# Performance work log

Hardware: AMD Instinct MI355X
Metric: run time of the kernel (lower is better)

The kernel has to match this reference:

```python
import jax, jax.numpy as jnp
import numpy as np

H = 2048          # hidden_size
I_MOE = 1408      # moe_intermediate_size (per expert)
I_SH = 5632       # shared_expert_intermediate_size
E = 8             # num_experts
TOP_K = 2         # num_experts_per_tok
B, S = 1, 2048


def setup_inputs() -> dict:
    key = jax.random.key(0)
    ks = jax.random.split(key, 7)
    sc = 0.02
    return {
        "hidden_states": jax.random.normal(ks[0], (B, S, H), jnp.float32),
        "W_router": jax.random.normal(ks[1], (E, H), jnp.float32) * sc,      # gate.weight
        "W_sgate": jax.random.normal(ks[2], (1, H), jnp.float32) * sc,       # shared_expert_gate.weight
        "Ws_gate_up": jax.random.normal(ks[3], (H, 2 * I_SH), jnp.float32) * sc,  # shared expert merged gate/up
        "Ws_down": jax.random.normal(ks[4], (I_SH, H), jnp.float32) * sc,
        "We_gate_up": jax.random.normal(ks[5], (E, H, 2 * I_MOE), jnp.float32) * sc,  # stacked expert gate/up
        "We_down": jax.random.normal(ks[6], (E, I_MOE, H), jnp.float32) * sc,
    }


def _silu_and_mul(gu, inter):
    # gate_up layout: [..., 2*inter] -> silu(gate) * up, matching SiluAndMul
    return jax.nn.silu(gu[..., :inter]) * gu[..., inter:]


def reference(hidden_states, W_router, W_sgate, Ws_gate_up, Ws_down, We_gate_up, We_down):
    orig_shape = hidden_states.shape
    x = hidden_states.reshape(-1, H)                     # [T, H]
    T = x.shape[0]

    # --- router: softmax in fp32 then top-k (NOT renormalized, as in source) ---
    logits = x @ W_router.T                              # [T, E]
    probs = jax.nn.softmax(logits.astype(jnp.float32), axis=-1)
    rw, sel = jax.lax.top_k(probs, TOP_K)                # [T, K]
    rw = rw.astype(x.dtype)

    # sparse combine matrix [T, E]: routing weight where selected, else 0
    combine = jnp.zeros((T, E), x.dtype).at[jnp.arange(T)[:, None], sel].add(rw)

    # --- shared expert ---
    sh = _silu_and_mul(x @ Ws_gate_up, I_SH) @ Ws_down    # [T, H]
    shared_out = sh * jax.nn.sigmoid(x @ W_sgate.T)       # [T, H]

    # --- experts: dense dispatch (math-identical to gather/MLP/index_add loop) ---
    gu = jnp.einsum('th,ehi->eti', x, We_gate_up)         # [E, T, 2*I_MOE]
    h = _silu_and_mul(gu, I_MOE)                          # [E, T, I_MOE]
    eo = jnp.einsum('eti,eih->eth', h, We_down)           # [E, T, H]
    sparse_out = jnp.einsum('eth,te->th', eo, combine)    # [T, H]

    return (shared_out + sparse_out).reshape(orig_shape)
```

## Files before the change

kernel.cpp:

```cpp
#include <hip/hip_runtime.h>
#include <cstdio>


#define H_DIM 2048
#define IMOE  1408
#define ISH   5632
#define NEXP  8
#define T_TOK 2048
#define TK_TOT (T_TOK * 2)

typedef __attribute__((ext_vector_type(8))) short short8;
typedef __attribute__((ext_vector_type(8))) __bf16 bf16x8;
typedef __attribute__((ext_vector_type(4))) float f32x4;

__device__ __forceinline__ float bf2f(unsigned short u) {
  union { unsigned int i; float f; } v; v.i = ((unsigned int)u) << 16; return v.f;
}
__device__ __forceinline__ unsigned short f2bf(float f) {
  union { float f; unsigned int i; } v; v.f = f;
  unsigned int x = v.i;
  return (unsigned short)((x + 0x7fffu + ((x >> 16) & 1u)) >> 16);
}

__device__ __forceinline__ f32x4 MFMA16(short8 a, short8 b, f32x4 c) {
  return __builtin_amdgcn_mfma_f32_16x16x32_bf16(
      __builtin_bit_cast(bf16x8, a), __builtin_bit_cast(bf16x8, b), c, 0, 0, 0);
}

__device__ __forceinline__ void gload_lds16(const unsigned short* g, unsigned short* l) {
  __builtin_amdgcn_global_load_lds(
      (const __attribute__((address_space(1))) unsigned int*)g,
      (__attribute__((address_space(3))) unsigned int*)l, 16, 0, 0);
}

__device__ __forceinline__ float silu_f(float x) { return x / (1.0f + __expf(-x)); }


__global__ __launch_bounds__(256)
void transpose_cvt_kernel(const float* __restrict__ src, unsigned short* __restrict__ dst,
                          int R, int C, long sStride, long dStride) {
  src += (long)blockIdx.z * sStride;
  dst += (long)blockIdx.z * dStride;
  __shared__ float tile[32][33];
  int tx = threadIdx.x, ty = threadIdx.y;
  int x = blockIdx.x * 32 + tx;
  int yb = blockIdx.y * 32;
#pragma unroll
  for (int j = 0; j < 4; j++) {
    int y = yb + ty + j * 8;
    tile[ty + j * 8][tx] = src[(long)y * C + x];
  }
  __syncthreads();
  int c = blockIdx.x * 32 + ty;
  int r = yb + tx;
#pragma unroll
  for (int j = 0; j < 4; j++) {
    dst[(long)(c + j * 8) * R + r] = f2bf(tile[tx][ty + j * 8]);
  }
}

__global__ __launch_bounds__(256)
void cvt_x_kernel(const float* __restrict__ x, unsigned short* __restrict__ xb, int total4) {
  int i = blockIdx.x * 256 + threadIdx.x;
  if (i >= total4) return;
  float4 v = ((const float4*)x)[i];
  ushort4 o;
  o.x = f2bf(v.x); o.y = f2bf(v.y); o.z = f2bf(v.z); o.w = f2bf(v.w);
  ((ushort4*)xb)[i] = o;
}


__global__ __launch_bounds__(256)
void router_kernel(const float* __restrict__ x, const float* __restrict__ Wr,
                   const float* __restrict__ Wsg, float* __restrict__ rw,
                   int* __restrict__ sel, float* __restrict__ sgate_sig,
                   int* __restrict__ counts) {
  int t = blockIdx.x;
  const float* xr = x + (long)t * H_DIM;
  float p[9];
#pragma unroll
  for (int e = 0; e < 9; e++) p[e] = 0.0f;
  for (int h = threadIdx.x; h < H_DIM; h += 256) {
    float xv = xr[h];
#pragma unroll
    for (int e = 0; e < 8; e++) p[e] += xv * Wr[e * H_DIM + h];
    p[8] += xv * Wsg[h];
  }
#pragma unroll
  for (int e = 0; e < 9; e++)
    for (int off = 32; off > 0; off >>= 1)
      p[e] += __shfl_down(p[e], off, 64);
  __shared__ float red[4][9];
  int wave = threadIdx.x >> 6, lane = threadIdx.x & 63;
  if (lane == 0) {
#pragma unroll
    for (int e = 0; e < 9; e++) red[wave][e] = p[e];
  }
  __syncthreads();
  if (threadIdx.x == 0) {
    float lg[9];
#pragma unroll
    for (int e = 0; e < 9; e++) lg[e] = red[0][e] + red[1][e] + red[2][e] + red[3][e];
    float m = lg[0];
#pragma unroll
    for (int e = 1; e < 8; e++) m = fmaxf(m, lg[e]);
    float pr[8], s = 0.0f;
#pragma unroll
    for (int e = 0; e < 8; e++) { pr[e] = expf(lg[e] - m); s += pr[e]; }
    float inv = 1.0f / s;
#pragma unroll
    for (int e = 0; e < 8; e++) pr[e] *= inv;
    int i0 = 0;
#pragma unroll
    for (int e = 1; e < 8; e++) if (pr[e] > pr[i0]) i0 = e;
    int i1 = (i0 == 0) ? 1 : 0;
#pragma unroll
    for (int e = 0; e < 8; e++) if (e != i0 && pr[e] > pr[i1]) i1 = e;
    rw[t * 2] = pr[i0]; rw[t * 2 + 1] = pr[i1];
    sel[t * 2] = i0;    sel[t * 2 + 1] = i1;
    sgate_sig[t] = 1.0f / (1.0f + expf(-lg[8]));
    atomicAdd(&counts[i0], 1);
    atomicAdd(&counts[i1], 1);
  }
}

__global__ void scan_kernel(const int* __restrict__ counts, int* __restrict__ offsets) {
  if (threadIdx.x == 0 && blockIdx.x == 0) {
    int s = 0;
    for (int e = 0; e < NEXP; e++) { offsets[e] = s; s += counts[e]; }
    offsets[NEXP] = s;
  }
}

__global__ __launch_bounds__(256)
void scatter_kernel(const int* __restrict__ sel, const int* __restrict__ offsets,
                    int* __restrict__ cursor, int* __restrict__ tok_of_slot,
                    int* __restrict__ slot_of_tok) {
  int t = blockIdx.x * 256 + threadIdx.x;
  if (t >= T_TOK) return;
#pragma unroll
  for (int k = 0; k < 2; k++) {
    int e = sel[t * 2 + k];
    int pos = atomicAdd(&cursor[e], 1);
    int slot = offsets[e] + pos;
    tok_of_slot[slot] = t;
    slot_of_tok[t * 2 + k] = slot;
  }
}

template <int EPI, bool EXPERT, bool GATHER>
__global__ __launch_bounds__(256, 2)
void gemm_bt_kernel(const unsigned short* __restrict__ A,
                    const unsigned short* __restrict__ BT,
                    void* __restrict__ Cv, int M, int N, int K,
                    const int* __restrict__ counts, const int* __restrict__ offsets,
                    const int* __restrict__ tok_of_slot,
                    const float* __restrict__ rowscale, long bt_estride) {
  int cnt = M, rowbase = 0;
  if constexpr (EXPERT) {
    int e = blockIdx.z;
    cnt = counts[e];
    rowbase = offsets[e];
    BT += (long)e * bt_estride;
  }
  int row0 = blockIdx.x * 128;
  if (row0 >= cnt) return;
  int col0 = blockIdx.y * 128;

  __shared__ unsigned short As[128 * 32];
  __shared__ unsigned short Bs[128 * 32];

  int tid = threadIdx.x;
  int wave = tid >> 6, lane = tid & 63;

  int c0 = wave * 64 + lane;
  int c1 = c0 + 256;
  int ar0 = c0 >> 2, ak0 = (c0 & 3) * 8;
  int ar1 = c1 >> 2, ak1 = (c1 & 3) * 8;

  long ga0, ga1;
  {
    int r0 = row0 + ar0, r1 = row0 + ar1;
    if constexpr (EXPERT) {
      int s0 = rowbase + min(r0, cnt - 1);
      int s1 = rowbase + min(r1, cnt - 1);
      if constexpr (GATHER) { ga0 = tok_of_slot[s0]; ga1 = tok_of_slot[s1]; }
      else { ga0 = s0; ga1 = s1; }
    } else { ga0 = r0; ga1 = r1; }
  }
  const unsigned short* aS0 = A + ga0 * (long)K + ak0;
  const unsigned short* aS1 = A + ga1 * (long)K + ak1;
  const unsigned short* bS0 = BT + (long)(col0 + ar0) * K + ak0;
  const unsigned short* bS1 = BT + (long)(col0 + ar1) * K + ak1;

  unsigned short* lA0 = &As[wave * 512];
  unsigned short* lA1 = &As[(4 + wave) * 512];
  unsigned short* lB0 = &Bs[wave * 512];
  unsigned short* lB1 = &Bs[(4 + wave) * 512];

  int wr = (wave >> 1) * 64, wc = (wave & 1) * 64;
  int fr = lane & 15, fg = lane >> 4;

  f32x4 acc[4][4] = {};

  for (int k = 0; k < K; k += 32) {
    gload_lds16(aS0 + k, lA0);
    gload_lds16(aS1 + k, lA1);
    gload_lds16(bS0 + k, lB0);
    gload_lds16(bS1 + k, lB1);
    __syncthreads();
    short8 aF[4], bF[4];
#pragma unroll
    for (int m = 0; m < 4; m++)
      aF[m] = *(const short8*)&As[(wr + m * 16 + fr) * 32 + fg * 8];
#pragma unroll
    for (int n = 0; n < 4; n++)
      bF[n] = *(const short8*)&Bs[(wc + n * 16 + fr) * 32 + fg * 8];
#pragma unroll
    for (int m = 0; m < 4; m++)
#pragma unroll
      for (int n = 0; n < 4; n++)
        acc[m][n] = MFMA16(aF[m], bF[n], acc[m][n]);
    __syncthreads();
  }

#pragma unroll
  for (int m = 0; m < 4; m++) {
    int rbase = wr + m * 16 + fg * 4;
#pragma unroll
    for (int n = 0; n < 4; n++) {
      int cg = col0 + wc + n * 16 + fr;
      f32x4 v = acc[m][n];
#pragma unroll
      for (int r = 0; r < 4; r++) {
        int rl = rbase + r;
        if (row0 + rl < cnt) {
          long orow = (long)(EXPERT ? rowbase : 0) + row0 + rl;
          long ci = orow * (long)N + cg;
          if constexpr (EPI == 0)      ((unsigned short*)Cv)[ci] = f2bf(v[r]);
          else if constexpr (EPI == 1) ((float*)Cv)[ci] = v[r] * rowscale[orow];
          else                         ((float*)Cv)[ci] = v[r];
        }
      }
    }
  }
}


__global__ __launch_bounds__(256)
void silu_mul_kernel(const unsigned short* __restrict__ gu, unsigned short* __restrict__ h,
                     int rows, int I) {
  int i = blockIdx.x * 256 + threadIdx.x;
  int i4 = I >> 2;
  if (i >= rows * i4) return;
  int row = i / i4;
  int ci = (i - row * i4) * 4;
  const unsigned short* g = gu + (long)row * 2 * I + ci;
  ushort4 gv = *(const ushort4*)g;
  ushort4 uv = *(const ushort4*)(g + I);
  ushort4 o;
  o.x = f2bf(silu_f(bf2f(gv.x)) * bf2f(uv.x));
  o.y = f2bf(silu_f(bf2f(gv.y)) * bf2f(uv.y));
  o.z = f2bf(silu_f(bf2f(gv.z)) * bf2f(uv.z));
  o.w = f2bf(silu_f(bf2f(gv.w)) * bf2f(uv.w));
  *(ushort4*)(h + (long)row * I + ci) = o;
}

__global__ __launch_bounds__(256)
void combine_kernel(float* __restrict__ out, const float* __restrict__ eo,
                    const int* __restrict__ slot_of_tok, const float* __restrict__ rw) {
  int i = blockIdx.x * 256 + threadIdx.x;
  const int h4n = H_DIM / 4;
  if (i >= T_TOK * h4n) return;
  int t = i / h4n;
  int h4 = i - t * h4n;
  int s0 = slot_of_tok[t * 2], s1 = slot_of_tok[t * 2 + 1];
  float w0 = rw[t * 2], w1 = rw[t * 2 + 1];
  float4 o = ((float4*)out)[i];
  float4 a = ((const float4*)eo)[(long)s0 * h4n + h4];
  float4 b = ((const float4*)eo)[(long)s1 * h4n + h4];
  o.x += w0 * a.x + w1 * b.x;
  o.y += w0 * a.y + w1 * b.y;
  o.z += w0 * a.z + w1 * b.z;
  o.w += w0 * a.w + w1 * b.w;
  ((float4*)out)[i] = o;
}


extern "C" void kernel_launch(void* const* d_in, const int* in_sizes, int n_in,
                              void* d_out, int out_size, void* d_ws, size_t ws_size,
                              hipStream_t stream) {
  (void)in_sizes; (void)n_in; (void)out_size;
  const float* x    = (const float*)d_in[0];
  const float* Wr   = (const float*)d_in[1];
  const float* Wsg  = (const float*)d_in[2];
  const float* Wsgu = (const float*)d_in[3];
  const float* Wsd  = (const float*)d_in[4];
  const float* Wegu = (const float*)d_in[5];
  const float* Wed  = (const float*)d_in[6];
  float* out = (float*)d_out;

  char* ws = (char*)d_ws;
  size_t off = 0;
  auto alloc = [&](size_t b) { size_t o = off; off += (b + 255) & ~(size_t)255; return o; };

  size_t o_xbf   = alloc((size_t)T_TOK * H_DIM * 2);
  size_t o_WsguT = alloc((size_t)2 * ISH * H_DIM * 2);
  size_t o_WsdT  = alloc((size_t)H_DIM * ISH * 2);
  size_t o_WeguT = alloc((size_t)NEXP * 2 * IMOE * H_DIM * 2);
  size_t o_WedT  = alloc((size_t)NEXP * H_DIM * IMOE * 2);
  size_t o_gush  = alloc((size_t)T_TOK * 2 * ISH * 2);
  size_t o_hsh   = alloc((size_t)T_TOK * ISH * 2);
  size_t o_ints  = alloc(256);
  size_t o_rw    = alloc((size_t)TK_TOT * 4);
  size_t o_sel   = alloc((size_t)TK_TOT * 4);
  size_t o_sg    = alloc((size_t)T_TOK * 4);
  size_t o_tok   = alloc((size_t)TK_TOT * 4);
  size_t o_s2t   = alloc((size_t)TK_TOT * 4);

  if (off > ws_size) {
    fprintf(stderr, "[moe kernel] workspace too small: need %zu have %zu\n", off, ws_size);
    return;
  }

  unsigned short* xbf   = (unsigned short*)(ws + o_xbf);
  unsigned short* WsguT = (unsigned short*)(ws + o_WsguT);
  unsigned short* WsdT  = (unsigned short*)(ws + o_WsdT);
  unsigned short* WeguT = (unsigned short*)(ws + o_WeguT);
  unsigned short* WedT  = (unsigned short*)(ws + o_WedT);
  unsigned short* gu_sh = (unsigned short*)(ws + o_gush);
  unsigned short* h_sh  = (unsigned short*)(ws + o_hsh);
  unsigned short* gu_e = (unsigned short*)(ws + o_gush);
  unsigned short* h_e  = (unsigned short*)(ws + o_gush + (size_t)TK_TOT * 2 * IMOE * 2);
  float* eo = (float*)(ws + o_WsguT);

  int* counts  = (int*)(ws + o_ints);
  int* cursor  = counts + 8;
  int* offsets = counts + 16;
  float* rw    = (float*)(ws + o_rw);
  int* sel     = (int*)(ws + o_sel);
  float* sgate = (float*)(ws + o_sg);
  int* tok     = (int*)(ws + o_tok);
  int* s2t     = (int*)(ws + o_s2t);

  dim3 tb(32, 8, 1);

  hipMemsetAsync(counts, 0, 64, stream);

  transpose_cvt_kernel<<<dim3(2 * ISH / 32, H_DIM / 32, 1), tb, 0, stream>>>(
      Wsgu, WsguT, H_DIM, 2 * ISH, 0, 0);
  transpose_cvt_kernel<<<dim3(H_DIM / 32, ISH / 32, 1), tb, 0, stream>>>(
      Wsd, WsdT, ISH, H_DIM, 0, 0);
  transpose_cvt_kernel<<<dim3(2 * IMOE / 32, H_DIM / 32, NEXP), tb, 0, stream>>>(
      Wegu, WeguT, H_DIM, 2 * IMOE, (long)H_DIM * 2 * IMOE, (long)2 * IMOE * H_DIM);
  transpose_cvt_kernel<<<dim3(H_DIM / 32, IMOE / 32, NEXP), tb, 0, stream>>>(
      Wed, WedT, IMOE, H_DIM, (long)IMOE * H_DIM, (long)H_DIM * IMOE);

  cvt_x_kernel<<<(T_TOK * H_DIM / 4) / 256, 256, 0, stream>>>(x, xbf, T_TOK * H_DIM / 4);

  router_kernel<<<T_TOK, 256, 0, stream>>>(x, Wr, Wsg, rw, sel, sgate, counts);
  scan_kernel<<<1, 64, 0, stream>>>(counts, offsets);
  scatter_kernel<<<(T_TOK + 255) / 256, 256, 0, stream>>>(sel, offsets, cursor, tok, s2t);

  gemm_bt_kernel<0, false, false><<<dim3(T_TOK / 128, 2 * ISH / 128, 1), 256, 0, stream>>>(
      xbf, WsguT, gu_sh, T_TOK, 2 * ISH, H_DIM, nullptr, nullptr, nullptr, nullptr, 0);
  silu_mul_kernel<<<(T_TOK * (ISH / 4)) / 256, 256, 0, stream>>>(gu_sh, h_sh, T_TOK, ISH);
  gemm_bt_kernel<1, false, false><<<dim3(T_TOK / 128, H_DIM / 128, 1), 256, 0, stream>>>(
      h_sh, WsdT, out, T_TOK, H_DIM, ISH, nullptr, nullptr, nullptr, sgate, 0);

  gemm_bt_kernel<0, true, true><<<dim3(T_TOK / 128, 2 * IMOE / 128, NEXP), 256, 0, stream>>>(
      xbf, WeguT, gu_e, T_TOK, 2 * IMOE, H_DIM, counts, offsets, tok, nullptr,
      (long)2 * IMOE * H_DIM);
  silu_mul_kernel<<<(TK_TOT * (IMOE / 4)) / 256, 256, 0, stream>>>(gu_e, h_e, TK_TOT, IMOE);
  gemm_bt_kernel<2, true, false><<<dim3(T_TOK / 128, H_DIM / 128, NEXP), 256, 0, stream>>>(
      h_e, WedT, eo, T_TOK, H_DIM, IMOE, counts, offsets, nullptr, nullptr,
      (long)H_DIM * IMOE);

  combine_kernel<<<(T_TOK * H_DIM / 4) / 256, 256, 0, stream>>>(out, eo, s2t, rw);
}
```

Baseline: 854.1 us.

## Replace GEMM with 256x256-tile, 4-stage pipelined, swizzled-LDS kernel and split-K down projection

Replaces the 128x128 single-buffered bf16 MFMA GEMM with a 512-thread kernel that computes 256x256 tiles. It uses a 4-deep global-to-LDS ring buffer with vmcnt-based waits, XOR-swizzled LDS addresses, and s_setprio around MFMA bursts. The aim is to raise operand reuse per LDS load and to hide global memory latency behind compute. The shared-expert down projection is split four ways along K and accumulated with float atomics into a zeroed output, which adds parallelism at the cost of an extra memset and atomic traffic. The 128KB LDS footprint limits occupancy to one block per CU.

```diff
diff --git a/kernel.cpp b/kernel.cpp
--- a/kernel.cpp
+++ b/kernel.cpp
@@ -34,6 +34,9 @@
 }
 
 __device__ __forceinline__ float silu_f(float x) { return x / (1.0f + __expf(-x)); }
+
+#define SBAR()   asm volatile("s_barrier" ::: "memory")
+#define VMCNT(n) asm volatile("s_waitcnt vmcnt(" #n ")" ::: "memory")
 
 
 __global__ __launch_bounds__(256)
@@ -149,97 +152,137 @@
 }
 
 template <int EPI, bool EXPERT, bool GATHER>
-__global__ __launch_bounds__(256, 2)
-void gemm_bt_kernel(const unsigned short* __restrict__ A,
-                    const unsigned short* __restrict__ BT,
-                    void* __restrict__ Cv, int M, int N, int K,
-                    const int* __restrict__ counts, const int* __restrict__ offsets,
-                    const int* __restrict__ tok_of_slot,
-                    const float* __restrict__ rowscale, long bt_estride) {
-  int cnt = M, rowbase = 0;
+__global__ __launch_bounds__(512, 2)
+void gemm8_kernel(const unsigned short* __restrict__ A,
+                  const unsigned short* __restrict__ BT,
+                  void* __restrict__ Cv,
+                  int N, int Kld, int KLEN, int M,
+                  const int* __restrict__ counts, const int* __restrict__ offsets,
+                  const int* __restrict__ tok_of_slot,
+                  const float* __restrict__ rowscale, long bt_estride) {
+  __shared__ unsigned short lds8[65536];
+
+  int cnt = M, rowbase = 0, k0 = 0;
+  const unsigned short* bt = BT;
   if constexpr (EXPERT) {
     int e = blockIdx.z;
     cnt = counts[e];
     rowbase = offsets[e];
-    BT += (long)e * bt_estride;
-  }
-  int row0 = blockIdx.x * 128;
+    bt += (long)e * bt_estride;
+  } else {
+    k0 = blockIdx.z * KLEN;
+  }
+  int row0 = blockIdx.x * 256;
   if (row0 >= cnt) return;
-  int col0 = blockIdx.y * 128;
-
-  __shared__ unsigned short As[128 * 32];
-  __shared__ unsigned short Bs[128 * 32];
-
-  int tid = threadIdx.x;
-  int wave = tid >> 6, lane = tid & 63;
-
-  int c0 = wave * 64 + lane;
-  int c1 = c0 + 256;
-  int ar0 = c0 >> 2, ak0 = (c0 & 3) * 8;
-  int ar1 = c1 >> 2, ak1 = (c1 & 3) * 8;
-
-  long ga0, ga1;
-  {
-    int r0 = row0 + ar0, r1 = row0 + ar1;
+  int col0 = blockIdx.y * 256;
+
+  int tid = threadIdx.x, wave = tid >> 6, lane = tid & 63;
+  int NT = KLEN / 32;
+
+  const unsigned short* aSrc[2];
+  const unsigned short* bSrc[2];
+#pragma unroll
+  for (int i = 0; i < 2; i++) {
+    int r = i * 128 + (tid >> 2);
+    int sw = (((tid & 3) ^ ((r >> 1) & 3)) * 8);
+    long arow;
     if constexpr (EXPERT) {
-      int s0 = rowbase + min(r0, cnt - 1);
-      int s1 = rowbase + min(r1, cnt - 1);
-      if constexpr (GATHER) { ga0 = tok_of_slot[s0]; ga1 = tok_of_slot[s1]; }
-      else { ga0 = s0; ga1 = s1; }
-    } else { ga0 = r0; ga1 = r1; }
-  }
-  const unsigned short* aS0 = A + ga0 * (long)K + ak0;
-  const unsigned short* aS1 = A + ga1 * (long)K + ak1;
-  const unsigned short* bS0 = BT + (long)(col0 + ar0) * K + ak0;
-  const unsigned short* bS1 = BT + (long)(col0 + ar1) * K + ak1;
-
-  unsigned short* lA0 = &As[wave * 512];
-  unsigned short* lA1 = &As[(4 + wave) * 512];
-  unsigned short* lB0 = &Bs[wave * 512];
-  unsigned short* lB1 = &Bs[(4 + wave) * 512];
-
-  int wr = (wave >> 1) * 64, wc = (wave & 1) * 64;
+      int s = rowbase + min(row0 + r, cnt - 1);
+      arow = GATHER ? tok_of_slot[s] : s;
+    } else {
+      arow = row0 + r;
+    }
+    aSrc[i] = A + arow * (long)Kld + k0 + sw;
+    bSrc[i] = bt + (long)(col0 + r) * Kld + k0 + sw;
+  }
+  int dA0 = wave * 512, dA1 = 4096 + wave * 512;
+  int dB0 = 8192 + wave * 512, dB1 = 12288 + wave * 512;
+
+  auto STAGE_A = [&](int u) {
+    int b2 = (u & 3) * 16384;
+    long kk = (long)min(u, NT - 1) * 32;
+    gload_lds16(aSrc[0] + kk, &lds8[b2 + dA0]);
+    gload_lds16(aSrc[1] + kk, &lds8[b2 + dA1]);
+  };
+  auto STAGE_B = [&](int u) {
+    int b2 = (u & 3) * 16384;
+    long kk = (long)min(u, NT - 1) * 32;
+    gload_lds16(bSrc[0] + kk, &lds8[b2 + dB0]);
+    gload_lds16(bSrc[1] + kk, &lds8[b2 + dB1]);
+  };
+
+  int wr = wave >> 2, wc = wave & 3;
   int fr = lane & 15, fg = lane >> 4;
-
-  f32x4 acc[4][4] = {};
-
-  for (int k = 0; k < K; k += 32) {
-    gload_lds16(aS0 + k, lA0);
-    gload_lds16(aS1 + k, lA1);
-    gload_lds16(bS0 + k, lB0);
-    gload_lds16(bS1 + k, lB1);
-    __syncthreads();
-    short8 aF[4], bF[4];
+  int addrA0[4], addrA1[4], addrB[4];
+#pragma unroll
+  for (int m = 0; m < 4; m++) {
+    int rl0 = wr * 128 + m * 16 + fr;
+    int rl1 = rl0 + 64;
+    int cl  = wc * 64 + m * 16 + fr;
+    addrA0[m] = rl0 * 32 + ((fg ^ ((rl0 >> 1) & 3)) * 8);
+    addrA1[m] = rl1 * 32 + ((fg ^ ((rl1 >> 1) & 3)) * 8);
+    addrB[m]  = 8192 + cl * 32 + ((fg ^ ((cl >> 1) & 3)) * 8);
+  }
+
+  STAGE_A(0); STAGE_B(0);
+  STAGE_A(1); STAGE_B(1);
+  STAGE_A(2); STAGE_B(2);
+  VMCNT(8);
+  SBAR();
+
+  f32x4 acc[8][4] = {};
+
+  for (int t = 0; t < NT; t++) {
+    int b = (t & 3) * 16384;
+    int u = t + 3;
+    short8 Bf[4], Af[4];
+#pragma unroll
+    for (int n = 0; n < 4; n++) Bf[n] = *(const short8*)&lds8[b + addrB[n]];
+#pragma unroll
+    for (int m = 0; m < 4; m++) Af[m] = *(const short8*)&lds8[b + addrA0[m]];
+    STAGE_A(u);
+    SBAR();
+    __builtin_amdgcn_s_setprio(1);
 #pragma unroll
     for (int m = 0; m < 4; m++)
-      aF[m] = *(const short8*)&As[(wr + m * 16 + fr) * 32 + fg * 8];
-#pragma unroll
-    for (int n = 0; n < 4; n++)
-      bF[n] = *(const short8*)&Bs[(wc + n * 16 + fr) * 32 + fg * 8];
+#pragma unroll
+      for (int n = 0; n < 4; n++)
+        acc[m][n] = MFMA16(Af[m], Bf[n], acc[m][n]);
+    __builtin_amdgcn_s_setprio(0);
+    SBAR();
+#pragma unroll
+    for (int m = 0; m < 4; m++) Af[m] = *(const short8*)&lds8[b + addrA1[m]];
+    STAGE_B(u);
+    SBAR();
+    __builtin_amdgcn_s_setprio(1);
 #pragma unroll
     for (int m = 0; m < 4; m++)
 #pragma unroll
       for (int n = 0; n < 4; n++)
-        acc[m][n] = MFMA16(aF[m], bF[n], acc[m][n]);
-    __syncthreads();
-  }
-
-#pragma unroll
-  for (int m = 0; m < 4; m++) {
-    int rbase = wr + m * 16 + fg * 4;
+        acc[4 + m][n] = MFMA16(Af[m], Bf[n], acc[4 + m][n]);
+    __builtin_amdgcn_s_setprio(0);
+    VMCNT(8);
+    SBAR();
+  }
+  VMCNT(0);
+
+  int rowguard = cnt - row0;
+#pragma unroll
+  for (int mq = 0; mq < 8; mq++) {
+    int rl = wr * 128 + (mq >> 2) * 64 + (mq & 3) * 16 + fg * 4;
 #pragma unroll
     for (int n = 0; n < 4; n++) {
-      int cg = col0 + wc + n * 16 + fr;
-      f32x4 v = acc[m][n];
-#pragma unroll
-      for (int r = 0; r < 4; r++) {
-        int rl = rbase + r;
-        if (row0 + rl < cnt) {
-          long orow = (long)(EXPERT ? rowbase : 0) + row0 + rl;
+      int cg = col0 + wc * 64 + n * 16 + fr;
+      f32x4 v = acc[mq][n];
+#pragma unroll
+      for (int j = 0; j < 4; j++) {
+        int r = rl + j;
+        if (r < rowguard) {
+          long orow = (long)rowbase + row0 + r;
           long ci = orow * (long)N + cg;
-          if constexpr (EPI == 0)      ((unsigned short*)Cv)[ci] = f2bf(v[r]);
-          else if constexpr (EPI == 1) ((float*)Cv)[ci] = v[r] * rowscale[orow];
-          else                         ((float*)Cv)[ci] = v[r];
+          if constexpr (EPI == 0)      ((unsigned short*)Cv)[ci] = f2bf(v[j]);
+          else if constexpr (EPI == 2) ((float*)Cv)[ci] = v[j];
+          else unsafeAtomicAdd(&((float*)Cv)[ci], v[j] * rowscale[orow]);
         }
       }
     }
@@ -362,19 +405,23 @@
   scan_kernel<<<1, 64, 0, stream>>>(counts, offsets);
   scatter_kernel<<<(T_TOK + 255) / 256, 256, 0, stream>>>(sel, offsets, cursor, tok, s2t);
 
-  gemm_bt_kernel<0, false, false><<<dim3(T_TOK / 128, 2 * ISH / 128, 1), 256, 0, stream>>>(
-      xbf, WsguT, gu_sh, T_TOK, 2 * ISH, H_DIM, nullptr, nullptr, nullptr, nullptr, 0);
+  gemm8_kernel<0, false, false><<<dim3(T_TOK / 256, 2 * ISH / 256, 1), 512, 0, stream>>>(
+      xbf, WsguT, gu_sh, 2 * ISH, H_DIM, H_DIM, T_TOK,
+      nullptr, nullptr, nullptr, nullptr, 0);
   silu_mul_kernel<<<(T_TOK * (ISH / 4)) / 256, 256, 0, stream>>>(gu_sh, h_sh, T_TOK, ISH);
-  gemm_bt_kernel<1, false, false><<<dim3(T_TOK / 128, H_DIM / 128, 1), 256, 0, stream>>>(
-      h_sh, WsdT, out, T_TOK, H_DIM, ISH, nullptr, nullptr, nullptr, sgate, 0);
-
-  gemm_bt_kernel<0, true, true><<<dim3(T_TOK / 128, 2 * IMOE / 128, NEXP), 256, 0, stream>>>(
-      xbf, WeguT, gu_e, T_TOK, 2 * IMOE, H_DIM, counts, offsets, tok, nullptr,
-      (long)2 * IMOE * H_DIM);
+
+  hipMemsetAsync(out, 0, (size_t)T_TOK * H_DIM * 4, stream);
+  gemm8_kernel<1, false, false><<<dim3(T_TOK / 256, H_DIM / 256, 4), 512, 0, stream>>>(
+      h_sh, WsdT, out, H_DIM, ISH, ISH / 4, T_TOK,
+      nullptr, nullptr, nullptr, sgate, 0);
+
+  gemm8_kernel<0, true, true><<<dim3(T_TOK / 256, 2 * IMOE / 256, NEXP), 512, 0, stream>>>(
+      xbf, WeguT, gu_e, 2 * IMOE, H_DIM, H_DIM, 0,
+      counts, offsets, tok, nullptr, (long)2 * IMOE * H_DIM);
   silu_mul_kernel<<<(TK_TOT * (IMOE / 4)) / 256, 256, 0, stream>>>(gu_e, h_e, TK_TOT, IMOE);
-  gemm_bt_kernel<2, true, false><<<dim3(T_TOK / 128, H_DIM / 128, NEXP), 256, 0, stream>>>(
-      h_e, WedT, eo, T_TOK, H_DIM, IMOE, counts, offsets, nullptr, nullptr,
-      (long)H_DIM * IMOE);
+  gemm8_kernel<2, true, false><<<dim3(T_TOK / 256, H_DIM / 256, NEXP), 512, 0, stream>>>(
+      h_e, WedT, eo, H_DIM, IMOE, IMOE, 0,
+      counts, offsets, nullptr, nullptr, (long)H_DIM * IMOE);
 
   combine_kernel<<<(T_TOK * H_DIM / 4) / 256, 256, 0, stream>>>(out, eo, s2t, rw);
 }
```

New measurement: 760.3 us. -11.0%, faster.

## Merge shared and expert GEMMs into grouped launches with split-K and LDS swizzle

Applied to the files above, without the earlier changes.

Shared-expert and routed-expert GEMMs are merged into a single grouped launch per phase, with an XCD-aware block remap, so both workloads fill the GPU at once. The gather of routed tokens moves into a separate pre-pass kernel. The shared down-projection uses split-K by 4 with atomic float adds into a zeroed output. LDS tiles get an XOR swizzle to cut bank conflicts, and the two SiLU kernels are fused into one. The cost is extra workspace, an output memset, atomics, and per-block branching in the kernel.

```diff
diff --git a/kernel.cpp b/kernel.cpp
--- a/kernel.cpp
+++ b/kernel.cpp
@@ -148,50 +148,78 @@
   }
 }
 
-template <int EPI, bool EXPERT, bool GATHER>
-__global__ __launch_bounds__(256, 2)
-void gemm_bt_kernel(const unsigned short* __restrict__ A,
-                    const unsigned short* __restrict__ BT,
-                    void* __restrict__ Cv, int M, int N, int K,
-                    const int* __restrict__ counts, const int* __restrict__ offsets,
-                    const int* __restrict__ tok_of_slot,
-                    const float* __restrict__ rowscale, long bt_estride) {
-  int cnt = M, rowbase = 0;
-  if constexpr (EXPERT) {
-    int e = blockIdx.z;
-    cnt = counts[e];
-    rowbase = offsets[e];
-    BT += (long)e * bt_estride;
-  }
-  int row0 = blockIdx.x * 128;
-  if (row0 >= cnt) return;
-  int col0 = blockIdx.y * 128;
+__global__ __launch_bounds__(256)
+void gather_kernel(const unsigned short* __restrict__ xbf, const int* __restrict__ tok,
+                   unsigned short* __restrict__ xg) {
+  int i = blockIdx.x * 256 + threadIdx.x;
+  int slot = i >> 8, c8 = i & 255;
+  long src = (long)tok[slot] * H_DIM + c8 * 8;
+  ulonglong2 v = *(const ulonglong2*)(xbf + src);
+  ((ulonglong2*)xg)[i] = v;
+}
+
+template <int PHASE>
+__global__ __launch_bounds__(256)
+void moe_gemm_kernel(const unsigned short* __restrict__ Ash,
+                     const unsigned short* __restrict__ Bsh,
+                     const unsigned short* __restrict__ Aex,
+                     const unsigned short* __restrict__ Bex,
+                     void* __restrict__ Csh, void* __restrict__ Cex,
+                     const int* __restrict__ counts,
+                     const int* __restrict__ offsets,
+                     const float* __restrict__ rowscale) {
+  int o = blockIdx.x;
+  int b = (o & 7) * (gridDim.x >> 3) + (o >> 3);
+
+  const unsigned short *A, *B;
+  char* Cc;
+  int N, Kld, nt, k0 = 0, row0, col0, rowbase = 0, cnt;
+  bool expert;
+  if constexpr (PHASE == 0) {
+    if (b < 1408) {
+      expert = false; A = Ash; B = Bsh; Cc = (char*)Csh;
+      N = 2 * ISH; Kld = H_DIM; nt = H_DIM / 32;
+      row0 = (b & 15) * 128; col0 = (b >> 4) * 128; cnt = T_TOK;
+    } else {
+      int b2 = b - 1408, e = b2 / 352, r2 = b2 % 352;
+      cnt = counts[e]; row0 = (r2 & 15) * 128;
+      if (row0 >= cnt) return;
+      rowbase = offsets[e];
+      expert = true; A = Aex; B = Bex + (long)e * 2 * IMOE * H_DIM; Cc = (char*)Cex;
+      N = 2 * IMOE; Kld = H_DIM; nt = H_DIM / 32;
+      col0 = (r2 >> 4) * 128;
+    }
+  } else {
+    if (b < 1024) {
+      expert = false; A = Ash; B = Bsh; Cc = (char*)Csh;
+      N = H_DIM; Kld = ISH; nt = (ISH / 4) / 32;
+      row0 = (b & 15) * 128; col0 = ((b >> 4) & 15) * 128; k0 = (b >> 8) * (ISH / 4);
+      cnt = T_TOK;
+    } else {
+      int b2 = b - 1024, e = b2 >> 8, r2 = b2 & 255;
+      cnt = counts[e]; row0 = (r2 & 15) * 128;
+      if (row0 >= cnt) return;
+      rowbase = offsets[e];
+      expert = true; A = Aex; B = Bex + (long)e * H_DIM * IMOE; Cc = (char*)Cex;
+      N = H_DIM; Kld = IMOE; nt = IMOE / 32;
+      col0 = (r2 >> 4) * 128;
+    }
+  }
 
   __shared__ unsigned short As[128 * 32];
   __shared__ unsigned short Bs[128 * 32];
 
-  int tid = threadIdx.x;
-  int wave = tid >> 6, lane = tid & 63;
-
-  int c0 = wave * 64 + lane;
-  int c1 = c0 + 256;
-  int ar0 = c0 >> 2, ak0 = (c0 & 3) * 8;
-  int ar1 = c1 >> 2, ak1 = (c1 & 3) * 8;
-
-  long ga0, ga1;
-  {
-    int r0 = row0 + ar0, r1 = row0 + ar1;
-    if constexpr (EXPERT) {
-      int s0 = rowbase + min(r0, cnt - 1);
-      int s1 = rowbase + min(r1, cnt - 1);
-      if constexpr (GATHER) { ga0 = tok_of_slot[s0]; ga1 = tok_of_slot[s1]; }
-      else { ga0 = s0; ga1 = s1; }
-    } else { ga0 = r0; ga1 = r1; }
-  }
-  const unsigned short* aS0 = A + ga0 * (long)K + ak0;
-  const unsigned short* aS1 = A + ga1 * (long)K + ak1;
-  const unsigned short* bS0 = BT + (long)(col0 + ar0) * K + ak0;
-  const unsigned short* bS1 = BT + (long)(col0 + ar1) * K + ak1;
+  int tid = threadIdx.x, wave = tid >> 6, lane = tid & 63;
+
+  int c0 = wave * 64 + lane, c1 = c0 + 256;
+  int ar0 = c0 >> 2, ar1 = c1 >> 2;
+  int ak0 = (((c0 & 3) ^ ((ar0 >> 1) & 3)) * 8);
+  int ak1 = (((c1 & 3) ^ ((ar1 >> 1) & 3)) * 8);
+
+  const unsigned short* aS0 = A + (long)(rowbase + min(row0 + ar0, cnt - 1)) * Kld + k0 + ak0;
+  const unsigned short* aS1 = A + (long)(rowbase + min(row0 + ar1, cnt - 1)) * Kld + k0 + ak1;
+  const unsigned short* bS0 = B + (long)(col0 + ar0) * Kld + k0 + ak0;
+  const unsigned short* bS1 = B + (long)(col0 + ar1) * Kld + k0 + ak1;
 
   unsigned short* lA0 = &As[wave * 512];
   unsigned short* lA1 = &As[(4 + wave) * 512];
@@ -200,22 +228,29 @@
 
   int wr = (wave >> 1) * 64, wc = (wave & 1) * 64;
   int fr = lane & 15, fg = lane >> 4;
+  int aAddr[4], bAddr[4];
+#pragma unroll
+  for (int m = 0; m < 4; m++) {
+    int r = wr + m * 16 + fr;
+    aAddr[m] = r * 32 + ((fg ^ ((r >> 1) & 3)) * 8);
+    int r2 = wc + m * 16 + fr;
+    bAddr[m] = r2 * 32 + ((fg ^ ((r2 >> 1) & 3)) * 8);
+  }
 
   f32x4 acc[4][4] = {};
 
-  for (int k = 0; k < K; k += 32) {
-    gload_lds16(aS0 + k, lA0);
-    gload_lds16(aS1 + k, lA1);
-    gload_lds16(bS0 + k, lB0);
-    gload_lds16(bS1 + k, lB1);
+  for (int t = 0; t < nt; t++) {
+    long kk = (long)t * 32;
+    gload_lds16(aS0 + kk, lA0);
+    gload_lds16(aS1 + kk, lA1);
+    gload_lds16(bS0 + kk, lB0);
+    gload_lds16(bS1 + kk, lB1);
     __syncthreads();
     short8 aF[4], bF[4];
 #pragma unroll
-    for (int m = 0; m < 4; m++)
-      aF[m] = *(const short8*)&As[(wr + m * 16 + fr) * 32 + fg * 8];
-#pragma unroll
-    for (int n = 0; n < 4; n++)
-      bF[n] = *(const short8*)&Bs[(wc + n * 16 + fr) * 32 + fg * 8];
+    for (int m = 0; m < 4; m++) aF[m] = *(const short8*)&As[aAddr[m]];
+#pragma unroll
+    for (int n = 0; n < 4; n++) bF[n] = *(const short8*)&Bs[bAddr[n]];
 #pragma unroll
     for (int m = 0; m < 4; m++)
 #pragma unroll
@@ -224,6 +259,7 @@
     __syncthreads();
   }
 
+  int rowguard = cnt - row0;
 #pragma unroll
   for (int m = 0; m < 4; m++) {
     int rbase = wr + m * 16 + fg * 4;
@@ -232,14 +268,17 @@
       int cg = col0 + wc + n * 16 + fr;
       f32x4 v = acc[m][n];
 #pragma unroll
-      for (int r = 0; r < 4; r++) {
-        int rl = rbase + r;
-        if (row0 + rl < cnt) {
-          long orow = (long)(EXPERT ? rowbase : 0) + row0 + rl;
+      for (int j = 0; j < 4; j++) {
+        int rl = rbase + j;
+        if (rl < rowguard) {
+          long orow = (long)rowbase + row0 + rl;
           long ci = orow * (long)N + cg;
-          if constexpr (EPI == 0)      ((unsigned short*)Cv)[ci] = f2bf(v[r]);
-          else if constexpr (EPI == 1) ((float*)Cv)[ci] = v[r] * rowscale[orow];
-          else                         ((float*)Cv)[ci] = v[r];
+          if constexpr (PHASE == 0) {
+            ((unsigned short*)Cc)[ci] = f2bf(v[j]);
+          } else {
+            if (!expert) unsafeAtomicAdd(&((float*)Cc)[ci], v[j] * rowscale[orow]);
+            else         ((float*)Cc)[ci] = v[j];
+          }
         }
       }
     }
@@ -248,22 +287,30 @@
 
 
 __global__ __launch_bounds__(256)
-void silu_mul_kernel(const unsigned short* __restrict__ gu, unsigned short* __restrict__ h,
-                     int rows, int I) {
+void silu2_kernel(const unsigned short* __restrict__ gu_sh, unsigned short* __restrict__ h_sh,
+                  const unsigned short* __restrict__ gu_e, unsigned short* __restrict__ h_e) {
   int i = blockIdx.x * 256 + threadIdx.x;
-  int i4 = I >> 2;
-  if (i >= rows * i4) return;
-  int row = i / i4;
-  int ci = (i - row * i4) * 4;
-  const unsigned short* g = gu + (long)row * 2 * I + ci;
-  ushort4 gv = *(const ushort4*)g;
-  ushort4 uv = *(const ushort4*)(g + I);
+  const int nsh = T_TOK * (ISH / 4);
+  const unsigned short* g;
+  unsigned short* h;
+  int I, row, c4;
+  if (i < nsh) {
+    g = gu_sh; h = h_sh; I = ISH;
+    row = i / (ISH / 4); c4 = i - row * (ISH / 4);
+  } else {
+    int j = i - nsh;
+    g = gu_e; h = h_e; I = IMOE;
+    row = j / (IMOE / 4); c4 = j - row * (IMOE / 4);
+  }
+  const unsigned short* gp = g + (long)row * 2 * I + c4 * 4;
+  ushort4 gv = *(const ushort4*)gp;
+  ushort4 uv = *(const ushort4*)(gp + I);
   ushort4 o;
   o.x = f2bf(silu_f(bf2f(gv.x)) * bf2f(uv.x));
   o.y = f2bf(silu_f(bf2f(gv.y)) * bf2f(uv.y));
   o.z = f2bf(silu_f(bf2f(gv.z)) * bf2f(uv.z));
   o.w = f2bf(silu_f(bf2f(gv.w)) * bf2f(uv.w));
-  *(ushort4*)(h + (long)row * I + ci) = o;
+  *(ushort4*)(h + (long)row * I + c4 * 4) = o;
 }
 
 __global__ __launch_bounds__(256)
@@ -311,6 +358,8 @@
   size_t o_WedT  = alloc((size_t)NEXP * H_DIM * IMOE * 2);
   size_t o_gush  = alloc((size_t)T_TOK * 2 * ISH * 2);
   size_t o_hsh   = alloc((size_t)T_TOK * ISH * 2);
+  size_t o_gue   = alloc((size_t)TK_TOT * 2 * IMOE * 2);
+  size_t o_xg    = alloc((size_t)TK_TOT * H_DIM * 2);
   size_t o_ints  = alloc(256);
   size_t o_rw    = alloc((size_t)TK_TOT * 4);
   size_t o_sel   = alloc((size_t)TK_TOT * 4);
@@ -330,9 +379,10 @@
   unsigned short* WedT  = (unsigned short*)(ws + o_WedT);
   unsigned short* gu_sh = (unsigned short*)(ws + o_gush);
   unsigned short* h_sh  = (unsigned short*)(ws + o_hsh);
-  unsigned short* gu_e = (unsigned short*)(ws + o_gush);
-  unsigned short* h_e  = (unsigned short*)(ws + o_gush + (size_t)TK_TOT * 2 * IMOE * 2);
-  float* eo = (float*)(ws + o_WsguT);
+  unsigned short* gu_e  = (unsigned short*)(ws + o_gue);
+  unsigned short* xg    = (unsigned short*)(ws + o_xg);
+  unsigned short* h_e   = (unsigned short*)(ws + o_WeguT);
+  float* eo             = (float*)(ws + o_WsguT);
 
   int* counts  = (int*)(ws + o_ints);
   int* cursor  = counts + 8;
@@ -346,6 +396,7 @@
   dim3 tb(32, 8, 1);
 
   hipMemsetAsync(counts, 0, 64, stream);
+  hipMemsetAsync(out, 0, (size_t)T_TOK * H_DIM * 4, stream);
 
   transpose_cvt_kernel<<<dim3(2 * ISH / 32, H_DIM / 32, 1), tb, 0, stream>>>(
       Wsgu, WsguT, H_DIM, 2 * ISH, 0, 0);
@@ -361,20 +412,18 @@
   router_kernel<<<T_TOK, 256, 0, stream>>>(x, Wr, Wsg, rw, sel, sgate, counts);
   scan_kernel<<<1, 64, 0, stream>>>(counts, offsets);
   scatter_kernel<<<(T_TOK + 255) / 256, 256, 0, stream>>>(sel, offsets, cursor, tok, s2t);
-
-  gemm_bt_kernel<0, false, false><<<dim3(T_TOK / 128, 2 * ISH / 128, 1), 256, 0, stream>>>(
-      xbf, WsguT, gu_sh, T_TOK, 2 * ISH, H_DIM, nullptr, nullptr, nullptr, nullptr, 0);
-  silu_mul_kernel<<<(T_TOK * (ISH / 4)) / 256, 256, 0, stream>>>(gu_sh, h_sh, T_TOK, ISH);
-  gemm_bt_kernel<1, false, false><<<dim3(T_TOK / 128, H_DIM / 128, 1), 256, 0, stream>>>(
-      h_sh, WsdT, out, T_TOK, H_DIM, ISH, nullptr, nullptr, nullptr, sgate, 0);
-
-  gemm_bt_kernel<0, true, true><<<dim3(T_TOK / 128, 2 * IMOE / 128, NEXP), 256, 0, stream>>>(
-      xbf, WeguT, gu_e, T_TOK, 2 * IMOE, H_DIM, counts, offsets, tok, nullptr,
-      (long)2 * IMOE * H_DIM);
-  silu_mul_kernel<<<(TK_TOT * (IMOE / 4)) / 256, 256, 0, stream>>>(gu_e, h_e, TK_TOT, IMOE);
-  gemm_bt_kernel<2, true, false><<<dim3(T_TOK / 128, H_DIM / 128, NEXP), 256, 0, stream>>>(
-      h_e, WedT, eo, T_TOK, H_DIM, IMOE, counts, offsets, nullptr, nullptr,
-      (long)H_DIM * IMOE);
+  gather_kernel<<<TK_TOT, 256, 0, stream>>>(xbf, tok, xg);
+
+  moe_gemm_kernel<0><<<4224, 256, 0, stream>>>(
+      xbf, WsguT, xg, WeguT, gu_sh, gu_e, counts, offsets, nullptr);
+
+  {
+    int total = T_TOK * (ISH / 4) + TK_TOT * (IMOE / 4);
+    silu2_kernel<<<total / 256, 256, 0, stream>>>(gu_sh, h_sh, gu_e, h_e);
+  }
+
+  moe_gemm_kernel<1><<<3072, 256, 0, stream>>>(
+      h_sh, WsdT, h_e, WedT, out, eo, counts, offsets, sgate);
 
   combine_kernel<<<(T_TOK * H_DIM / 4) / 256, 256, 0, stream>>>(out, eo, s2t, rw);
 }
```

After: 1.012 ms. +18.5%, slower.
